# Performance work log

Hardware: AMD Instinct MI355X
Metric: run time of the kernel (lower is better)

Reference implementation:

```python
import jax, jax.numpy as jnp
import numpy as np

D_MODEL = 1024
N_HEADS = 16
D_KEY = D_MODEL // N_HEADS
NEG = -1e9


def setup_inputs() -> dict:
    key = jax.random.key(0)
    ks = jax.random.split(key, 10)
    B, S = 4, 2048
    s = 0.02
    query = jax.random.normal(ks[0], (B, S, D_MODEL), dtype=jnp.float32)
    # causal mask: 1 where attend allowed, 0 where masked (masked_fill(mask==0, -1e9))
    mask = jnp.tril(jnp.ones((S, S), dtype=jnp.int32))[None, None]
    Wq = jax.random.normal(ks[1], (D_MODEL, D_MODEL), dtype=jnp.float32) * s
    bq = jax.random.normal(ks[2], (D_MODEL,), dtype=jnp.float32) * s
    Wk = jax.random.normal(ks[3], (D_MODEL, D_MODEL), dtype=jnp.float32) * s
    bk = jax.random.normal(ks[4], (D_MODEL,), dtype=jnp.float32) * s
    Wv = jax.random.normal(ks[5], (D_MODEL, D_MODEL), dtype=jnp.float32) * s
    bv = jax.random.normal(ks[6], (D_MODEL,), dtype=jnp.float32) * s
    Wo = jax.random.normal(ks[7], (D_MODEL, D_MODEL), dtype=jnp.float32) * s
    bo = jax.random.normal(ks[8], (D_MODEL,), dtype=jnp.float32) * s
    return {"query": query, "mask": mask, "Wq": Wq, "bq": bq, "Wk": Wk,
            "bk": bk, "Wv": Wv, "bv": bv, "Wo": Wo, "bo": bo}


def _split_heads(x):
    B, S, _ = x.shape
    return x.reshape(B, S, N_HEADS, D_KEY).transpose(0, 2, 1, 3)  # [B,H,S,Dk]


def reference(query, mask, Wq, bq, Wk, bk, Wv, bv, Wo, bo):
    B, S, _ = query.shape
    # torch Linear: x @ W^T + b
    q = _split_heads(query @ Wq.T + bq)
    k = _split_heads(query @ Wk.T + bk)  # self-attention: key_value is None
    v = _split_heads(query @ Wv.T + bv)
    scores = jnp.einsum('bhqd,bhkd->bhqk', q, k) / jnp.sqrt(jnp.float32(D_KEY))
    scores = jnp.where(mask == 0, jnp.float32(NEG), scores)
    weights = jax.nn.softmax(scores, axis=-1)  # dropout=0 (eval)
    attn = jnp.einsum('bhqk,bhkd->bhqd', weights, v)
    merged = attn.transpose(0, 2, 1, 3).reshape(B, S, D_MODEL)
    return merged @ Wo.T + bo
```

## Files before the change

### kernel.cpp

```cpp
#include <hip/hip_runtime.h>
#include <hip/hip_bf16.h>

typedef __attribute__((ext_vector_type(8))) short bf16x8;
typedef __attribute__((ext_vector_type(4))) float f32x4;
typedef __attribute__((ext_vector_type(16))) float f32x16;
typedef __attribute__((ext_vector_type(2))) unsigned int u32x2;

__device__ __forceinline__ float fexp2(float x) { return __builtin_amdgcn_exp2f(x); }

__device__ __forceinline__ ushort f2bf(float x) {
    union { float f; unsigned u; } c; c.f = x;
    unsigned r = c.u + 0x7fff + ((c.u >> 16) & 1);
    return (ushort)(r >> 16);
}

__device__ __forceinline__ unsigned cvtpk(float lo, float hi) {
    unsigned r;
    asm("v_cvt_pk_bf16_f32 %0, %1, %2" : "=v"(r) : "v"(lo), "v"(hi));
    return r;
}

__device__ __forceinline__ void gload16(const void* g, void* l) {
    __builtin_amdgcn_global_load_lds((const __attribute__((address_space(1))) void*)g,
                                     (__attribute__((address_space(3))) void*)l, 16, 0, 0);
}

__device__ __forceinline__ void blockbar() {
    asm volatile("" ::: "memory");
    __builtin_amdgcn_s_barrier();
    asm volatile("" ::: "memory");
}

__global__ void cvt_all(const float* __restrict__ X, const float* __restrict__ wa,
                        const float* __restrict__ wb, const float* __restrict__ wc,
                        const float* __restrict__ wd,
                        ushort* __restrict__ oX, ushort* __restrict__ oWcat,
                        ushort* __restrict__ oWo) {
    const int NX4 = 2097152;
    const int NW4 = 262144;
    const int TOT = NX4 + 4 * NW4;
    int i = blockIdx.x * blockDim.x + threadIdx.x;
    int stride = gridDim.x * blockDim.x;
    for (; i < TOT; i += stride) {
        const float* src; ushort4* dst; int local;
        if (i < NX4) { src = X; local = i; dst = (ushort4*)oX; }
        else {
            int j = i - NX4, sel = j >> 18; local = j & (NW4 - 1);
            src = (sel == 0) ? wa : (sel == 1) ? wb : (sel == 2) ? wc : wd;
            dst = (sel < 3) ? (ushort4*)oWcat + sel * NW4 : (ushort4*)oWo;
        }
        float4 v = ((const float4*)src)[local];
        ushort4 o;
        o.x = f2bf(v.x); o.y = f2bf(v.y); o.z = f2bf(v.z); o.w = f2bf(v.w);
        dst[local] = o;
    }
}

template<int MODE>
__global__ __launch_bounds__(512, 2)
void gemm_p2(const ushort* __restrict__ A, const ushort* __restrict__ Bt,
             const float* __restrict__ bias0, const float* __restrict__ bias1,
             const float* __restrict__ bias2,
             ushort* __restrict__ outb, float* __restrict__ outf,
             int M, int N, int K) {
    __shared__ ushort lds[49152];
    const int t = threadIdx.x, lane = t & 63, w = t >> 6;
    const int wm = w >> 1, wn = w & 1;
    const int l15 = lane & 15, lg = lane >> 4;
    const int sw7 = l15 & 7;

    const int nbx = N >> 7;
    const int nwg = nbx * (M >> 8);
    const int bid = blockIdx.y * nbx + blockIdx.x;
    const int swz = (bid & 7) * (nwg >> 3) + (bid >> 3);
    const int m0 = (swz / nbx) * 256, n0 = (swz % nbx) * 128;

    const int srow = lane >> 3;
    const int gcb = (lane & 7) ^ srow;
    const ushort* gsrc[6];
#pragma unroll
    for (int s = 0; s < 4; s++)
        gsrc[s] = A + (size_t)(m0 + s * 64 + w * 8 + srow) * K + gcb * 8;
#pragma unroll
    for (int s = 0; s < 2; s++)
        gsrc[4 + s] = Bt + (size_t)(n0 + s * 64 + w * 8 + srow) * K + gcb * 8;

#define STAGE(ST, KT) { \
    ushort* dst = &lds[(ST) * 24576 + w * 512]; \
    gload16(gsrc[0] + (KT) * 64, dst); \
    gload16(gsrc[1] + (KT) * 64, dst + 4096); \
    gload16(gsrc[2] + (KT) * 64, dst + 8192); \
    gload16(gsrc[3] + (KT) * 64, dst + 12288); \
    gload16(gsrc[4] + (KT) * 64, dst + 16384); \
    gload16(gsrc[5] + (KT) * 64, dst + 20480); }

    f32x4 acc[4][4] = {};
    const int NT = K >> 6;

    STAGE(0, 0); STAGE(1, 1);

    for (int kt = 0; kt < NT; ++kt) {
        if (kt < NT - 1) asm volatile("s_waitcnt vmcnt(6)" ::: "memory");
        else             asm volatile("s_waitcnt vmcnt(0)" ::: "memory");
        blockbar();

        const ushort* stg = &lds[(kt & 1) * 24576];
        bf16x8 a0[4], b0[4], a1[4], b1[4];
#pragma unroll
        for (int mi = 0; mi < 4; mi++) {
            int row = wm * 64 + mi * 16 + l15;
            a0[mi] = *(const bf16x8*)&stg[row * 64 + ((lg ^ sw7) << 3)];
            a1[mi] = *(const bf16x8*)&stg[row * 64 + (((4 + lg) ^ sw7) << 3)];
        }
#pragma unroll
        for (int ni = 0; ni < 4; ni++) {
            int row = wn * 64 + ni * 16 + l15;
            b0[ni] = *(const bf16x8*)&stg[16384 + row * 64 + ((lg ^ sw7) << 3)];
            b1[ni] = *(const bf16x8*)&stg[16384 + row * 64 + (((4 + lg) ^ sw7) << 3)];
        }

        __builtin_amdgcn_s_setprio(1);
#pragma unroll
        for (int mi = 0; mi < 4; mi++)
#pragma unroll
            for (int ni = 0; ni < 4; ni++)
                acc[mi][ni] = __builtin_amdgcn_mfma_f32_16x16x32_bf16(a0[mi], b0[ni], acc[mi][ni], 0, 0, 0);
        __builtin_amdgcn_s_setprio(0);

        asm volatile("s_waitcnt lgkmcnt(0)" ::: "memory");
        blockbar();
        if (kt + 2 < NT) STAGE((kt & 1), kt + 2);

        __builtin_amdgcn_s_setprio(1);
#pragma unroll
        for (int mi = 0; mi < 4; mi++)
#pragma unroll
            for (int ni = 0; ni < 4; ni++)
                acc[mi][ni] = __builtin_amdgcn_mfma_f32_16x16x32_bf16(a1[mi], b1[ni], acc[mi][ni], 0, 0, 0);
        __builtin_amdgcn_s_setprio(0);
    }
#undef STAGE

#pragma unroll
    for (int mi = 0; mi < 4; mi++)
#pragma unroll
        for (int ni = 0; ni < 4; ni++)
#pragma unroll
            for (int r = 0; r < 4; r++) {
                int gm = m0 + wm * 64 + mi * 16 + lg * 4 + r;
                int gn = n0 + wn * 64 + ni * 16 + l15;
                if (MODE == 0) {
                    const float* bp = (gn < 1024) ? bias0 : ((gn < 2048) ? bias1 : bias2);
                    float v = acc[mi][ni][r] + bp[gn & 1023];
                    if (gn < 1024) v *= 0.18033688011f;
                    int proj = gn >> 10, nn = gn & 1023;
                    int h = nn >> 6, d = nn & 63;
                    int b = gm >> 11, s = gm & 2047;
                    outb[(size_t)proj * 8388608 + ((((size_t)b << 4) + h) * 2048 + s) * 64 + d] = f2bf(v);
                } else {
                    outf[(size_t)gm * N + gn] = acc[mi][ni][r] + bias0[gn];
                }
            }
}

__global__ __launch_bounds__(256, 4)
void attn_fwd(const ushort* __restrict__ Qb, const ushort* __restrict__ Kb,
              const ushort* __restrict__ Vb, ushort* __restrict__ Ab) {
    constexpr int S = 2048;
    __shared__ ushort lds[16384];

    const int bid = blockIdx.x;
    const int qt = 15 - (bid >> 6);
    const int bh = bid & 63;
    const int b = bh >> 4, h = bh & 15;
    const ushort* Qp = Qb + (size_t)bh * S * 64;
    const ushort* Kp = Kb + (size_t)bh * S * 64;
    const ushort* Vp = Vb + (size_t)bh * S * 64;

    const int t = threadIdx.x, lane = t & 63, w = t >> 6;
    const int l15 = lane & 15, l31 = lane & 31, hi = lane >> 5, g = lane >> 4;

    int koff[2], voff[2];
#pragma unroll
    for (int i = 0; i < 2; i++) {
        int row = (w * 2 + i) * 8 + (lane >> 3);
        int gg = (lane & 7) ^ ((row ^ (row >> 3)) & 7);
        koff[i] = row * 64 + gg * 8;
    }
#pragma unroll
    for (int it = 0; it < 2; it++) {
        int T = (it * 4 + w) * 64 + lane;
        int kvb = T >> 5, db = (T >> 3) & 3, kvr = (T >> 1) & 3, dh = T & 1;
        voff[it] = (kvb * 4 + kvr) * 64 + db * 16 + dh * 8;
    }
    const unsigned vtbase = (unsigned)(uintptr_t)&lds[8192]
                          + (hi << 10) + ((g & 1) << 7) + (l15 << 3);

    auto stage = [&](int phase, int k0) {
#pragma unroll
        for (int i = 0; i < 2; i++)
            gload16(Kp + (size_t)k0 * 64 + koff[i], &lds[(phase << 12) + ((w * 2 + i) << 9)]);
#pragma unroll
        for (int it = 0; it < 2; it++)
            gload16(Vp + (size_t)k0 * 64 + voff[it], &lds[8192 + (phase << 12) + (((it << 2) + w) << 9)]);
    };

    const int fb = qt * 128 + w * 32;
    const int nt = 2 * qt + 2;

    bf16x8 qf[4];
#pragma unroll
    for (int kc = 0; kc < 4; kc++)
        qf[kc] = *(const bf16x8*)&Qp[(size_t)(fb + l31) * 64 + kc * 16 + hi * 8];

    float m = -3e38f, ls = 0.f;
    f32x16 O0 = {}, O1 = {};

    stage(0, 0);

    for (int tile = 0; tile < nt; tile++) {
        const int phase = tile & 1;
        const int k0 = tile * 64;
        asm volatile("s_waitcnt vmcnt(0)" ::: "memory");
        blockbar();
        if (tile + 1 < nt) stage(phase ^ 1, (tile + 1) * 64);

        if (k0 <= fb + 31) {
            const ushort* Kc = &lds[phase << 12];
            f32x16 s0 = {}, s1 = {};
            {
                bf16x8 kf[4];
#pragma unroll
                for (int kc = 0; kc < 4; kc++) {
                    int row = l31;
                    int sw = (row ^ (row >> 3)) & 7;
                    kf[kc] = *(const bf16x8*)&Kc[row * 64 + (((kc * 2 + hi) ^ sw) << 3)];
                }
                __builtin_amdgcn_s_setprio(1);
#pragma unroll
                for (int kc = 0; kc < 4; kc++)
                    s0 = __builtin_amdgcn_mfma_f32_32x32x16_bf16(kf[kc], qf[kc], s0, 0, 0, 0);
                __builtin_amdgcn_s_setprio(0);
            }
            {
                bf16x8 kf[4];
#pragma unroll
                for (int kc = 0; kc < 4; kc++) {
                    int row = 32 + l31;
                    int sw = (row ^ (row >> 3)) & 7;
                    kf[kc] = *(const bf16x8*)&Kc[row * 64 + (((kc * 2 + hi) ^ sw) << 3)];
                }
                __builtin_amdgcn_s_setprio(1);
#pragma unroll
                for (int kc = 0; kc < 4; kc++)
                    s1 = __builtin_amdgcn_mfma_f32_32x32x16_bf16(kf[kc], qf[kc], s1, 0, 0, 0);
                __builtin_amdgcn_s_setprio(0);
            }

            float pv[32];
            const bool diag = (k0 + 63 > fb);
            const int rel = fb + l31 - k0 - 4 * hi;
#pragma unroll
            for (int r = 0; r < 16; r++) {
                float v0 = s0[r], v1 = s1[r];
                if (diag) {
                    int kvc = (r & 3) + 8 * (r >> 2);
                    if (kvc > rel)      v0 = -1e30f;
                    if (kvc + 32 > rel) v1 = -1e30f;
                }
                pv[r] = v0; pv[16 + r] = v1;
            }
            float mx[16];
#pragma unroll
            for (int i = 0; i < 16; i++) mx[i] = fmaxf(pv[i], pv[i + 16]);
#pragma unroll
            for (int sgap = 8; sgap >= 1; sgap >>= 1)
#pragma unroll
                for (int i = 0; i < sgap; i++) mx[i] = fmaxf(mx[i], mx[i + sgap]);
            float pmax = fmaxf(mx[0], __shfl_xor(mx[0], 32));

            if (!__all(pmax <= m + 8.f)) {
                float mnew = fmaxf(m, pmax);
                float a = fexp2(m - mnew);
                ls *= a;
                float ar[16];
#pragma unroll
                for (int r = 0; r < 16; r++)
                    ar[r] = __shfl(a, (r & 3) + 8 * (r >> 2) + 4 * hi, 32);
#pragma unroll
                for (int r = 0; r < 16; r++) { O0[r] *= ar[r]; O1[r] *= ar[r]; }
                m = mnew;
            }
#pragma unroll
            for (int i = 0; i < 32; i++) pv[i] = fexp2(pv[i] - m);
            float sm[16];
#pragma unroll
            for (int i = 0; i < 16; i++) sm[i] = pv[i] + pv[i + 16];
#pragma unroll
            for (int sgap = 8; sgap >= 1; sgap >>= 1)
#pragma unroll
                for (int i = 0; i < sgap; i++) sm[i] += sm[i + sgap];
            ls += sm[0] + __shfl_xor(sm[0], 32);

            union PAu { bf16x8 v; unsigned wd[4]; } PA[4];
#pragma unroll
            for (int ks = 0; ks < 4; ks++)
#pragma unroll
                for (int i = 0; i < 2; i++) {
                    unsigned xw = cvtpk(pv[8 * ks + 2 * i], pv[8 * ks + 2 * i + 1]);
                    unsigned yw = cvtpk(pv[8 * ks + 2 * i + 4], pv[8 * ks + 2 * i + 5]);
                    asm("v_permlane32_swap_b32 %0, %1" : "+v"(xw), "+v"(yw));
                    PA[ks].wd[i] = xw; PA[ks].wd[2 + i] = yw;
                }

            const unsigned vtb = vtbase + (phase << 13);
            u32x2 vb[16];
#define TRR(idx, OFFSTR) asm volatile("ds_read_b64_tr_b16 %0, %1 offset:" OFFSTR : "=v"(vb[idx]) : "v"(vtb))
            TRR(0, "0");    TRR(1, "512");  TRR(2, "2048"); TRR(3, "2560");
            TRR(4, "4096"); TRR(5, "4608"); TRR(6, "6144"); TRR(7, "6656");
            TRR(8, "256");  TRR(9, "768");  TRR(10, "2304"); TRR(11, "2816");
            TRR(12, "4352"); TRR(13, "4864"); TRR(14, "6400"); TRR(15, "6912");
#undef TRR
            union FragU { bf16x8 v; u32x2 hh[2]; };
            asm volatile("s_waitcnt lgkmcnt(8)" ::: "memory");
            __builtin_amdgcn_sched_barrier(0);
            __builtin_amdgcn_s_setprio(1);
#pragma unroll
            for (int ks = 0; ks < 4; ks++) {
                FragU f; f.hh[0] = vb[ks * 2]; f.hh[1] = vb[ks * 2 + 1];
                O0 = __builtin_amdgcn_mfma_f32_32x32x16_bf16(PA[ks].v, f.v, O0, 0, 0, 0);
            }
            __builtin_amdgcn_s_setprio(0);
            asm volatile("s_waitcnt lgkmcnt(0)" ::: "memory");
            __builtin_amdgcn_sched_barrier(0);
            __builtin_amdgcn_s_setprio(1);
#pragma unroll
            for (int ks = 0; ks < 4; ks++) {
                FragU f; f.hh[0] = vb[8 + ks * 2]; f.hh[1] = vb[8 + ks * 2 + 1];
                O1 = __builtin_amdgcn_mfma_f32_32x32x16_bf16(PA[ks].v, f.v, O1, 0, 0, 0);
            }
            __builtin_amdgcn_s_setprio(0);
        }
    }

    float inv[16];
#pragma unroll
    for (int r = 0; r < 16; r++)
        inv[r] = __builtin_amdgcn_rcpf(__shfl(ls, (r & 3) + 8 * (r >> 2) + 4 * hi, 32));
#pragma unroll
    for (int r = 0; r < 16; r++) {
        int q = fb + (r & 3) + 8 * (r >> 2) + 4 * hi;
        size_t base = ((size_t)b * 2048 + q) * 1024 + h * 64;
        Ab[base + l31]      = f2bf(O0[r] * inv[r]);
        Ab[base + 32 + l31] = f2bf(O1[r] * inv[r]);
    }
}

extern "C" void kernel_launch(void* const* d_in, const int* in_sizes, int n_in,
                              void* d_out, int out_size, void* d_ws, size_t ws_size,
                              hipStream_t stream) {
    const float* query = (const float*)d_in[0];
    const float* Wq = (const float*)d_in[2];
    const float* bq = (const float*)d_in[3];
    const float* Wk = (const float*)d_in[4];
    const float* bk = (const float*)d_in[5];
    const float* Wv = (const float*)d_in[6];
    const float* bv = (const float*)d_in[7];
    const float* Wo = (const float*)d_in[8];
    const float* bo = (const float*)d_in[9];
    float* out = (float*)d_out;

    char* ws = (char*)d_ws;
    const size_t SZ_X = 8192ull * 1024 * 2;
    const size_t SZ_W = 1024ull * 1024 * 2;
    ushort* Xb   = (ushort*)(ws);
    ushort* Wcat = (ushort*)(ws + SZ_X);
    ushort* Wob  = (ushort*)(ws + SZ_X + 3 * SZ_W);
    ushort* QKVb = (ushort*)(ws + SZ_X + 4 * SZ_W);
    ushort* Ab   = (ushort*)(ws + 4 * SZ_X + 4 * SZ_W);

    cvt_all<<<2048, 256, 0, stream>>>(query, Wq, Wk, Wv, Wo, Xb, Wcat, Wob);

    gemm_p2<0><<<dim3(3072 / 128, 8192 / 256), 512, 0, stream>>>(
        Xb, Wcat, bq, bk, bv, QKVb, nullptr, 8192, 3072, 1024);

    attn_fwd<<<1024, 256, 0, stream>>>(QKVb, QKVb + 8388608, QKVb + 2 * 8388608, Ab);

    gemm_p2<1><<<dim3(1024 / 128, 8192 / 256), 512, 0, stream>>>(
        Ab, Wob, bo, nullptr, nullptr, nullptr, out, 8192, 1024, 1024);
}
```

Baseline: 163.4 us.

## Use BK=32 GEMM variant with half LDS for QKV projection

```diff
diff --git a/kernel.cpp b/kernel.cpp
--- a/kernel.cpp
+++ b/kernel.cpp
@@ -57,17 +57,16 @@
 }
 
 template<int MODE>
-__global__ __launch_bounds__(512, 2)
-void gemm_p2(const ushort* __restrict__ A, const ushort* __restrict__ Bt,
-             const float* __restrict__ bias0, const float* __restrict__ bias1,
-             const float* __restrict__ bias2,
-             ushort* __restrict__ outb, float* __restrict__ outf,
-             int M, int N, int K) {
-    __shared__ ushort lds[49152];
+__global__ __launch_bounds__(512, 4)
+void gemm_bk32(const ushort* __restrict__ A, const ushort* __restrict__ Bt,
+               const float* __restrict__ bias0, const float* __restrict__ bias1,
+               const float* __restrict__ bias2,
+               ushort* __restrict__ outb, float* __restrict__ outf,
+               int M, int N, int K) {
+    __shared__ ushort lds[24576];
     const int t = threadIdx.x, lane = t & 63, w = t >> 6;
     const int wm = w >> 1, wn = w & 1;
     const int l15 = lane & 15, lg = lane >> 4;
-    const int sw7 = l15 & 7;
 
     const int nbx = N >> 7;
     const int nwg = nbx * (M >> 8);
@@ -75,48 +74,40 @@
     const int swz = (bid & 7) * (nwg >> 3) + (bid >> 3);
     const int m0 = (swz / nbx) * 256, n0 = (swz % nbx) * 128;
 
-    const int srow = lane >> 3;
-    const int gcb = (lane & 7) ^ srow;
-    const ushort* gsrc[6];
-#pragma unroll
-    for (int s = 0; s < 4; s++)
-        gsrc[s] = A + (size_t)(m0 + s * 64 + w * 8 + srow) * K + gcb * 8;
-#pragma unroll
-    for (int s = 0; s < 2; s++)
-        gsrc[4 + s] = Bt + (size_t)(n0 + s * 64 + w * 8 + srow) * K + gcb * 8;
+    const int rA0 = t >> 2, pcb = t & 3;
+    const int rA1 = rA0 + 128;
+    const int gA0 = pcb ^ ((rA0 >> 1) & 3);
+    const int gA1 = pcb ^ ((rA1 >> 1) & 3);
+    const ushort* srcA0 = A + (size_t)(m0 + rA0) * K + gA0 * 8;
+    const ushort* srcA1 = A + (size_t)(m0 + rA1) * K + gA1 * 8;
+    const ushort* srcB  = Bt + (size_t)(n0 + rA0) * K + gA0 * 8;
 
 #define STAGE(ST, KT) { \
-    ushort* dst = &lds[(ST) * 24576 + w * 512]; \
-    gload16(gsrc[0] + (KT) * 64, dst); \
-    gload16(gsrc[1] + (KT) * 64, dst + 4096); \
-    gload16(gsrc[2] + (KT) * 64, dst + 8192); \
-    gload16(gsrc[3] + (KT) * 64, dst + 12288); \
-    gload16(gsrc[4] + (KT) * 64, dst + 16384); \
-    gload16(gsrc[5] + (KT) * 64, dst + 20480); }
+    gload16(srcA0 + (KT) * 32, &lds[(ST) * 12288 + t * 8]); \
+    gload16(srcA1 + (KT) * 32, &lds[(ST) * 12288 + 4096 + t * 8]); \
+    gload16(srcB  + (KT) * 32, &lds[(ST) * 12288 + 8192 + t * 8]); }
 
     f32x4 acc[4][4] = {};
-    const int NT = K >> 6;
+    const int NT = K >> 5;
 
     STAGE(0, 0); STAGE(1, 1);
 
     for (int kt = 0; kt < NT; ++kt) {
-        if (kt < NT - 1) asm volatile("s_waitcnt vmcnt(6)" ::: "memory");
+        if (kt < NT - 1) asm volatile("s_waitcnt vmcnt(3)" ::: "memory");
         else             asm volatile("s_waitcnt vmcnt(0)" ::: "memory");
         blockbar();
 
-        const ushort* stg = &lds[(kt & 1) * 24576];
-        bf16x8 a0[4], b0[4], a1[4], b1[4];
+        const ushort* stg = &lds[(kt & 1) * 12288];
+        bf16x8 af[4], bfr[4];
 #pragma unroll
         for (int mi = 0; mi < 4; mi++) {
             int row = wm * 64 + mi * 16 + l15;
-            a0[mi] = *(const bf16x8*)&stg[row * 64 + ((lg ^ sw7) << 3)];
-            a1[mi] = *(const bf16x8*)&stg[row * 64 + (((4 + lg) ^ sw7) << 3)];
+            af[mi] = *(const bf16x8*)&stg[row * 32 + ((lg ^ ((row >> 1) & 3)) << 3)];
         }
 #pragma unroll
         for (int ni = 0; ni < 4; ni++) {
             int row = wn * 64 + ni * 16 + l15;
-            b0[ni] = *(const bf16x8*)&stg[16384 + row * 64 + ((lg ^ sw7) << 3)];
-            b1[ni] = *(const bf16x8*)&stg[16384 + row * 64 + (((4 + lg) ^ sw7) << 3)];
+            bfr[ni] = *(const bf16x8*)&stg[8192 + row * 32 + ((lg ^ ((row >> 1) & 3)) << 3)];
         }
 
         __builtin_amdgcn_s_setprio(1);
@@ -124,20 +115,12 @@
         for (int mi = 0; mi < 4; mi++)
 #pragma unroll
             for (int ni = 0; ni < 4; ni++)
-                acc[mi][ni] = __builtin_amdgcn_mfma_f32_16x16x32_bf16(a0[mi], b0[ni], acc[mi][ni], 0, 0, 0);
+                acc[mi][ni] = __builtin_amdgcn_mfma_f32_16x16x32_bf16(af[mi], bfr[ni], acc[mi][ni], 0, 0, 0);
         __builtin_amdgcn_s_setprio(0);
 
         asm volatile("s_waitcnt lgkmcnt(0)" ::: "memory");
         blockbar();
         if (kt + 2 < NT) STAGE((kt & 1), kt + 2);
-
-        __builtin_amdgcn_s_setprio(1);
-#pragma unroll
-        for (int mi = 0; mi < 4; mi++)
-#pragma unroll
-            for (int ni = 0; ni < 4; ni++)
-                acc[mi][ni] = __builtin_amdgcn_mfma_f32_16x16x32_bf16(a1[mi], b1[ni], acc[mi][ni], 0, 0, 0);
-        __builtin_amdgcn_s_setprio(0);
     }
 #undef STAGE
 
@@ -163,6 +146,113 @@
             }
 }
 
+template<int MODE>
+__global__ __launch_bounds__(512, 2)
+void gemm_p2(const ushort* __restrict__ A, const ushort* __restrict__ Bt,
+             const float* __restrict__ bias0, const float* __restrict__ bias1,
+             const float* __restrict__ bias2,
+             ushort* __restrict__ outb, float* __restrict__ outf,
+             int M, int N, int K) {
+    __shared__ ushort lds[49152];
+    const int t = threadIdx.x, lane = t & 63, w = t >> 6;
+    const int wm = w >> 1, wn = w & 1;
+    const int l15 = lane & 15, lg = lane >> 4;
+    const int sw7 = l15 & 7;
+
+    const int nbx = N >> 7;
+    const int nwg = nbx * (M >> 8);
+    const int bid = blockIdx.y * nbx + blockIdx.x;
+    const int swz = (bid & 7) * (nwg >> 3) + (bid >> 3);
+    const int m0 = (swz / nbx) * 256, n0 = (swz % nbx) * 128;
+
+    const int srow = lane >> 3;
+    const int gcb = (lane & 7) ^ srow;
+    const ushort* gsrc[6];
+#pragma unroll
+    for (int s = 0; s < 4; s++)
+        gsrc[s] = A + (size_t)(m0 + s * 64 + w * 8 + srow) * K + gcb * 8;
+#pragma unroll
+    for (int s = 0; s < 2; s++)
+        gsrc[4 + s] = Bt + (size_t)(n0 + s * 64 + w * 8 + srow) * K + gcb * 8;
+
+#define STAGE(ST, KT) { \
+    ushort* dst = &lds[(ST) * 24576 + w * 512]; \
+    gload16(gsrc[0] + (KT) * 64, dst); \
+    gload16(gsrc[1] + (KT) * 64, dst + 4096); \
+    gload16(gsrc[2] + (KT) * 64, dst + 8192); \
+    gload16(gsrc[3] + (KT) * 64, dst + 12288); \
+    gload16(gsrc[4] + (KT) * 64, dst + 16384); \
+    gload16(gsrc[5] + (KT) * 64, dst + 20480); }
+
+    f32x4 acc[4][4] = {};
+    const int NT = K >> 6;
+
+    STAGE(0, 0); STAGE(1, 1);
+
+    for (int kt = 0; kt < NT; ++kt) {
+        if (kt < NT - 1) asm volatile("s_waitcnt vmcnt(6)" ::: "memory");
+        else             asm volatile("s_waitcnt vmcnt(0)" ::: "memory");
+        blockbar();
+
+        const ushort* stg = &lds[(kt & 1) * 24576];
+        bf16x8 a0[4], b0[4], a1[4], b1[4];
+#pragma unroll
+        for (int mi = 0; mi < 4; mi++) {
+            int row = wm * 64 + mi * 16 + l15;
+            a0[mi] = *(const bf16x8*)&stg[row * 64 + ((lg ^ sw7) << 3)];
+            a1[mi] = *(const bf16x8*)&stg[row * 64 + (((4 + lg) ^ sw7) << 3)];
+        }
+#pragma unroll
+        for (int ni = 0; ni < 4; ni++) {
+            int row = wn * 64 + ni * 16 + l15;
+            b0[ni] = *(const bf16x8*)&stg[16384 + row * 64 + ((lg ^ sw7) << 3)];
+            b1[ni] = *(const bf16x8*)&stg[16384 + row * 64 + (((4 + lg) ^ sw7) << 3)];
+        }
+
+        __builtin_amdgcn_s_setprio(1);
+#pragma unroll
+        for (int mi = 0; mi < 4; mi++)
+#pragma unroll
+            for (int ni = 0; ni < 4; ni++)
+                acc[mi][ni] = __builtin_amdgcn_mfma_f32_16x16x32_bf16(a0[mi], b0[ni], acc[mi][ni], 0, 0, 0);
+        __builtin_amdgcn_s_setprio(0);
+
+        asm volatile("s_waitcnt lgkmcnt(0)" ::: "memory");
+        blockbar();
+        if (kt + 2 < NT) STAGE((kt & 1), kt + 2);
+
+        __builtin_amdgcn_s_setprio(1);
+#pragma unroll
+        for (int mi = 0; mi < 4; mi++)
+#pragma unroll
+            for (int ni = 0; ni < 4; ni++)
+                acc[mi][ni] = __builtin_amdgcn_mfma_f32_16x16x32_bf16(a1[mi], b1[ni], acc[mi][ni], 0, 0, 0);
+        __builtin_amdgcn_s_setprio(0);
+    }
+#undef STAGE
+
+#pragma unroll
+    for (int mi = 0; mi < 4; mi++)
+#pragma unroll
+        for (int ni = 0; ni < 4; ni++)
+#pragma unroll
+            for (int r = 0; r < 4; r++) {
+                int gm = m0 + wm * 64 + mi * 16 + lg * 4 + r;
+                int gn = n0 + wn * 64 + ni * 16 + l15;
+                if (MODE == 0) {
+                    const float* bp = (gn < 1024) ? bias0 : ((gn < 2048) ? bias1 : bias2);
+                    float v = acc[mi][ni][r] + bp[gn & 1023];
+                    if (gn < 1024) v *= 0.18033688011f;
+                    int proj = gn >> 10, nn = gn & 1023;
+                    int h = nn >> 6, d = nn & 63;
+                    int b = gm >> 11, s = gm & 2047;
+                    outb[(size_t)proj * 8388608 + ((((size_t)b << 4) + h) * 2048 + s) * 64 + d] = f2bf(v);
+                } else {
+                    outf[(size_t)gm * N + gn] = acc[mi][ni][r] + bias0[gn];
+                }
+            }
+}
+
 __global__ __launch_bounds__(256, 4)
 void attn_fwd(const ushort* __restrict__ Qb, const ushort* __restrict__ Kb,
               const ushort* __restrict__ Vb, ushort* __restrict__ Ab) {
@@ -257,19 +347,19 @@
                 __builtin_amdgcn_s_setprio(0);
             }
 
+            const bool diag = (k0 + 63 > fb);
+            if (diag) {
+                const int rel = fb + l31 - k0 - 4 * hi;
+#pragma unroll
+                for (int r = 0; r < 16; r++) {
+                    int kvc = (r & 3) + 8 * (r >> 2);
+                    if (kvc > rel)      s0[r] = -1e30f;
+                    if (kvc + 32 > rel) s1[r] = -1e30f;
+                }
+            }
             float pv[32];
-            const bool diag = (k0 + 63 > fb);
-            const int rel = fb + l31 - k0 - 4 * hi;
-#pragma unroll
-            for (int r = 0; r < 16; r++) {
-                float v0 = s0[r], v1 = s1[r];
-                if (diag) {
-                    int kvc = (r & 3) + 8 * (r >> 2);
-                    if (kvc > rel)      v0 = -1e30f;
-                    if (kvc + 32 > rel) v1 = -1e30f;
-                }
-                pv[r] = v0; pv[16 + r] = v1;
-            }
+#pragma unroll
+            for (int r = 0; r < 16; r++) { pv[r] = s0[r]; pv[16 + r] = s1[r]; }
             float mx[16];
 #pragma unroll
             for (int i = 0; i < 16; i++) mx[i] = fmaxf(pv[i], pv[i + 16]);
@@ -381,7 +471,7 @@
 
     cvt_all<<<2048, 256, 0, stream>>>(query, Wq, Wk, Wv, Wo, Xb, Wcat, Wob);
 
-    gemm_p2<0><<<dim3(3072 / 128, 8192 / 256), 512, 0, stream>>>(
+    gemm_bk32<0><<<dim3(3072 / 128, 8192 / 256), 512, 0, stream>>>(
         Xb, Wcat, bq, bk, bv, QKVb, nullptr, 8192, 3072, 1024);
 
     attn_fwd<<<1024, 256, 0, stream>>>(QKVb, QKVb + 8388608, QKVb + 2 * 8388608, Ab);
```

Result: faster. 154.4 us (-5.5%).

## Restructure GEMM into 3-stage LDS ring with K=32 tiles and one barrier

Applied to the files above, without the earlier changes.

```diff
diff --git a/kernel.cpp b/kernel.cpp
--- a/kernel.cpp
+++ b/kernel.cpp
@@ -57,17 +57,16 @@
 }
 
 template<int MODE>
-__global__ __launch_bounds__(512, 2)
-void gemm_p2(const ushort* __restrict__ A, const ushort* __restrict__ Bt,
-             const float* __restrict__ bias0, const float* __restrict__ bias1,
-             const float* __restrict__ bias2,
-             ushort* __restrict__ outb, float* __restrict__ outf,
-             int M, int N, int K) {
-    __shared__ ushort lds[49152];
+__global__ __launch_bounds__(512, 4)
+void gemm_ring(const ushort* __restrict__ A, const ushort* __restrict__ Bt,
+               const float* __restrict__ bias0, const float* __restrict__ bias1,
+               const float* __restrict__ bias2,
+               ushort* __restrict__ outb, float* __restrict__ outf,
+               int M, int N, int K) {
+    __shared__ ushort lds[36864];
     const int t = threadIdx.x, lane = t & 63, w = t >> 6;
     const int wm = w >> 1, wn = w & 1;
     const int l15 = lane & 15, lg = lane >> 4;
-    const int sw7 = l15 & 7;
 
     const int nbx = N >> 7;
     const int nwg = nbx * (M >> 8);
@@ -75,68 +74,50 @@
     const int swz = (bid & 7) * (nwg >> 3) + (bid >> 3);
     const int m0 = (swz / nbx) * 256, n0 = (swz % nbx) * 128;
 
-    const int srow = lane >> 3;
-    const int gcb = (lane & 7) ^ srow;
-    const ushort* gsrc[6];
-#pragma unroll
-    for (int s = 0; s < 4; s++)
-        gsrc[s] = A + (size_t)(m0 + s * 64 + w * 8 + srow) * K + gcb * 8;
-#pragma unroll
-    for (int s = 0; s < 2; s++)
-        gsrc[4 + s] = Bt + (size_t)(n0 + s * 64 + w * 8 + srow) * K + gcb * 8;
+    const int rA0 = t >> 2, pcb = t & 3;
+    const int rA1 = rA0 + 128;
+    const int gA0 = pcb ^ ((rA0 >> 1) & 3);
+    const int gA1 = pcb ^ ((rA1 >> 1) & 3);
+    const ushort* srcA0 = A + (size_t)(m0 + rA0) * K + gA0 * 8;
+    const ushort* srcA1 = A + (size_t)(m0 + rA1) * K + gA1 * 8;
+    const ushort* srcB  = Bt + (size_t)(n0 + rA0) * K + gA0 * 8;
 
 #define STAGE(ST, KT) { \
-    ushort* dst = &lds[(ST) * 24576 + w * 512]; \
-    gload16(gsrc[0] + (KT) * 64, dst); \
-    gload16(gsrc[1] + (KT) * 64, dst + 4096); \
-    gload16(gsrc[2] + (KT) * 64, dst + 8192); \
-    gload16(gsrc[3] + (KT) * 64, dst + 12288); \
-    gload16(gsrc[4] + (KT) * 64, dst + 16384); \
-    gload16(gsrc[5] + (KT) * 64, dst + 20480); }
+    gload16(srcA0 + (KT) * 32, &lds[(ST) * 12288 + t * 8]); \
+    gload16(srcA1 + (KT) * 32, &lds[(ST) * 12288 + 4096 + t * 8]); \
+    gload16(srcB  + (KT) * 32, &lds[(ST) * 12288 + 8192 + t * 8]); }
 
     f32x4 acc[4][4] = {};
-    const int NT = K >> 6;
+    const int NT = K >> 5;
 
     STAGE(0, 0); STAGE(1, 1);
 
     for (int kt = 0; kt < NT; ++kt) {
-        if (kt < NT - 1) asm volatile("s_waitcnt vmcnt(6)" ::: "memory");
+        if (kt < NT - 1) asm volatile("s_waitcnt vmcnt(3)" ::: "memory");
         else             asm volatile("s_waitcnt vmcnt(0)" ::: "memory");
         blockbar();
 
-        const ushort* stg = &lds[(kt & 1) * 24576];
-        bf16x8 a0[4], b0[4], a1[4], b1[4];
+        const ushort* stg = &lds[(kt % 3) * 12288];
+        bf16x8 af[4], bfr[4];
 #pragma unroll
         for (int mi = 0; mi < 4; mi++) {
             int row = wm * 64 + mi * 16 + l15;
-            a0[mi] = *(const bf16x8*)&stg[row * 64 + ((lg ^ sw7) << 3)];
-            a1[mi] = *(const bf16x8*)&stg[row * 64 + (((4 + lg) ^ sw7) << 3)];
+            af[mi] = *(const bf16x8*)&stg[row * 32 + ((lg ^ ((row >> 1) & 3)) << 3)];
         }
 #pragma unroll
         for (int ni = 0; ni < 4; ni++) {
             int row = wn * 64 + ni * 16 + l15;
-            b0[ni] = *(const bf16x8*)&stg[16384 + row * 64 + ((lg ^ sw7) << 3)];
-            b1[ni] = *(const bf16x8*)&stg[16384 + row * 64 + (((4 + lg) ^ sw7) << 3)];
+            bfr[ni] = *(const bf16x8*)&stg[8192 + row * 32 + ((lg ^ ((row >> 1) & 3)) << 3)];
         }
 
+        if (kt + 2 < NT) STAGE((kt + 2) % 3, kt + 2);
+
         __builtin_amdgcn_s_setprio(1);
 #pragma unroll
         for (int mi = 0; mi < 4; mi++)
 #pragma unroll
             for (int ni = 0; ni < 4; ni++)
-                acc[mi][ni] = __builtin_amdgcn_mfma_f32_16x16x32_bf16(a0[mi], b0[ni], acc[mi][ni], 0, 0, 0);
-        __builtin_amdgcn_s_setprio(0);
-
-        asm volatile("s_waitcnt lgkmcnt(0)" ::: "memory");
-        blockbar();
-        if (kt + 2 < NT) STAGE((kt & 1), kt + 2);
-
-        __builtin_amdgcn_s_setprio(1);
-#pragma unroll
-        for (int mi = 0; mi < 4; mi++)
-#pragma unroll
-            for (int ni = 0; ni < 4; ni++)
-                acc[mi][ni] = __builtin_amdgcn_mfma_f32_16x16x32_bf16(a1[mi], b1[ni], acc[mi][ni], 0, 0, 0);
+                acc[mi][ni] = __builtin_amdgcn_mfma_f32_16x16x32_bf16(af[mi], bfr[ni], acc[mi][ni], 0, 0, 0);
         __builtin_amdgcn_s_setprio(0);
     }
 #undef STAGE
@@ -257,19 +238,19 @@
                 __builtin_amdgcn_s_setprio(0);
             }
 
+            const bool diag = (k0 + 63 > fb);
+            if (diag) {
+                const int rel = fb + l31 - k0 - 4 * hi;
+#pragma unroll
+                for (int r = 0; r < 16; r++) {
+                    int kvc = (r & 3) + 8 * (r >> 2);
+                    if (kvc > rel)      s0[r] = -1e30f;
+                    if (kvc + 32 > rel) s1[r] = -1e30f;
+                }
+            }
             float pv[32];
-            const bool diag = (k0 + 63 > fb);
-            const int rel = fb + l31 - k0 - 4 * hi;
-#pragma unroll
-            for (int r = 0; r < 16; r++) {
-                float v0 = s0[r], v1 = s1[r];
-                if (diag) {
-                    int kvc = (r & 3) + 8 * (r >> 2);
-                    if (kvc > rel)      v0 = -1e30f;
-                    if (kvc + 32 > rel) v1 = -1e30f;
-                }
-                pv[r] = v0; pv[16 + r] = v1;
-            }
+#pragma unroll
+            for (int r = 0; r < 16; r++) { pv[r] = s0[r]; pv[16 + r] = s1[r]; }
             float mx[16];
 #pragma unroll
             for (int i = 0; i < 16; i++) mx[i] = fmaxf(pv[i], pv[i + 16]);
@@ -381,11 +362,11 @@
 
     cvt_all<<<2048, 256, 0, stream>>>(query, Wq, Wk, Wv, Wo, Xb, Wcat, Wob);
 
-    gemm_p2<0><<<dim3(3072 / 128, 8192 / 256), 512, 0, stream>>>(
+    gemm_ring<0><<<dim3(3072 / 128, 8192 / 256), 512, 0, stream>>>(
         Xb, Wcat, bq, bk, bv, QKVb, nullptr, 8192, 3072, 1024);
 
     attn_fwd<<<1024, 256, 0, stream>>>(QKVb, QKVb + 8388608, QKVb + 2 * 8388608, Ab);
 
-    gemm_p2<1><<<dim3(1024 / 128, 8192 / 256), 512, 0, stream>>>(
+    gemm_ring<1><<<dim3(1024 / 128, 8192 / 256), 512, 0, stream>>>(
         Ab, Wob, bo, nullptr, nullptr, nullptr, out, 8192, 1024, 1024);
 }
```

New measurement: 153.4 us. 1.07x faster.
